# Performance work log

Hardware: AMD Instinct MI355X
Metric: run time of the kernel (lower is better)

Reference implementation:

```python
import jax, jax.numpy as jnp
import numpy as np

B, S, D = 8, 1024, 768
H = 12
DH = D // H  # 64


def setup_inputs() -> dict:
    key = jax.random.key(0)
    k1, k2 = jax.random.split(key)
    x = jax.random.normal(k1, (B, S, D), dtype=jnp.float32)
    attention_mask = jnp.zeros((B, 1, 1, S), dtype=jnp.float32)
    W = jax.random.normal(k2, (D, D), dtype=jnp.float32) * (1.0 / np.sqrt(D))
    b = jnp.zeros((D,), dtype=jnp.float32)
    return {"x": x, "attention_mask": attention_mask, "W": W, "b": b}


def reference(x, attention_mask, W, b):
    # Linear projection (torch Linear: y = x @ W^T + b; here W is [out,in])
    mixed = jnp.einsum('bsd,ed->bse', x, W) + b            # [B,S,D]
    # split heads -> [B,H,S,DH]
    xl = mixed.reshape(B, S, H, DH).transpose(0, 2, 1, 3)
    # self-attention with Q=K=V=xl
    scores = jnp.einsum('bhsd,bhtd->bhst', xl, xl) / jnp.sqrt(
        jnp.asarray(DH, dtype=xl.dtype))                    # [B,H,S,S]
    scores = scores + attention_mask
    probs = jax.nn.softmax(scores, axis=-1)
    ctx = jnp.einsum('bhst,bhtd->bhsd', probs, xl)          # [B,H,S,DH]
    ctx = ctx.transpose(0, 2, 1, 3).reshape(B, S, D)        # [B,S,D]
    return ctx
```

## Files before the change

kernel.cpp:

```cpp
#include <hip/hip_runtime.h>
#include <hip/hip_bf16.h>


#define D_MODEL 768
#define SEQ     1024
#define NHEAD   12
#define DHEAD   64
#define BATCH   8
#define QB      128
#define LOG2E   1.44269504088896f
#define FMLOG   28.8539008178f
#define SCLC    (0.125f * LOG2E)

typedef __attribute__((ext_vector_type(8)))  short bf16x8;
typedef __attribute__((ext_vector_type(4)))  short short4v;
typedef __attribute__((ext_vector_type(4)))  float f32x4;
typedef __attribute__((ext_vector_type(16))) float f32x16;

__device__ __forceinline__ unsigned short f2bf(float f) {
  __hip_bfloat16 h = __float2bfloat16(f);
  return *reinterpret_cast<unsigned short*>(&h);
}

__device__ __forceinline__ float fexp2(float x) {
#if __has_builtin(__builtin_amdgcn_exp2f)
  return __builtin_amdgcn_exp2f(x);
#else
  return exp2f(x);
#endif
}

__device__ __forceinline__ int lswz(int r, int c) {
  return (r << 6) + (c ^ ((r & 7) << 3));
}
__device__ __forceinline__ int tau(int t) {
  return (t & ~0xC) | ((t & 8) >> 1) | ((t & 4) << 1);
}

template<bool WRITE_T>
__global__ __launch_bounds__(256) void proj_kernel(
    const float* __restrict__ X, const float* __restrict__ W,
    const float* __restrict__ bias, unsigned short* __restrict__ mixed,
    unsigned short* __restrict__ mixedT)
{
  __shared__ unsigned short As[2][64 * 40];
  __shared__ unsigned short Bs[2][128 * 40];

  const int tid = threadIdx.x;
  const int l   = tid & 63;
  const int w   = tid >> 6;
  const int m0  = blockIdx.x * 64;
  const int n0  = blockIdx.y * 128;
  const int wm  = (w >> 1) * 32;
  const int wn  = (w & 1) * 64;
  const int lr  = l & 15;
  const int g   = l >> 4;
  const int lk  = g * 8;

  const int ar = tid >> 2;
  const int ac = (tid & 3) * 8;

  f32x4 a0, a1, b0[2], b1[2];
  auto loadSlab = [&](int k0) {
    const float* pa = &X[(size_t)(m0 + ar) * D_MODEL + k0 + ac];
    a0 = *(const f32x4*)pa;
    a1 = *(const f32x4*)(pa + 4);
    #pragma unroll
    for (int p = 0; p < 2; ++p) {
      const float* pb = &W[(size_t)(n0 + ar + p * 64) * D_MODEL + k0 + ac];
      b0[p] = *(const f32x4*)pb;
      b1[p] = *(const f32x4*)(pb + 4);
    }
  };
  auto stageSlab = [&](int bb) {
    bf16x8 av;
    #pragma unroll
    for (int jj = 0; jj < 4; ++jj) {
      av[jj]     = (short)f2bf(a0[jj]);
      av[4 + jj] = (short)f2bf(a1[jj]);
    }
    *(bf16x8*)&As[bb][ar * 40 + ac] = av;
    #pragma unroll
    for (int p = 0; p < 2; ++p) {
      bf16x8 bv;
      #pragma unroll
      for (int jj = 0; jj < 4; ++jj) {
        bv[jj]     = (short)f2bf(b0[p][jj]);
        bv[4 + jj] = (short)f2bf(b1[p][jj]);
      }
      *(bf16x8*)&Bs[bb][(ar + p * 64) * 40 + ac] = bv;
    }
  };

  f32x4 acc[2][4] = {};

  loadSlab(0);
  stageSlab(0);
  __syncthreads();

  int cur = 0;
  for (int k0 = 0; k0 < D_MODEL; k0 += 32) {
    const bool more = (k0 + 32 < D_MODEL);
    if (more) loadSlab(k0 + 32);

    bf16x8 af[2], bfr[4];
    #pragma unroll
    for (int am = 0; am < 2; ++am)
      af[am]  = *(const bf16x8*)&As[cur][(wm + am * 16 + lr) * 40 + lk];
    #pragma unroll
    for (int bn = 0; bn < 4; ++bn)
      bfr[bn] = *(const bf16x8*)&Bs[cur][(wn + bn * 16 + lr) * 40 + lk];

    #pragma unroll
    for (int am = 0; am < 2; ++am)
      #pragma unroll
      for (int bn = 0; bn < 4; ++bn)
        acc[am][bn] = __builtin_amdgcn_mfma_f32_16x16x32_bf16(
            af[am], bfr[bn], acc[am][bn], 0, 0, 0);

    if (more) {
      stageSlab(cur ^ 1);
      __syncthreads();
    }
    cur ^= 1;
  }

  const int orow = g * 4;
  const int bT   = m0 >> 10;
  const int tl0  = (m0 & 1023) + wm + orow;
  #pragma unroll
  for (int bn = 0; bn < 4; ++bn) {
    int   col  = n0 + wn + bn * 16 + lr;
    float bcol = bias[col];
    size_t tbase = ((size_t)bT * D_MODEL + col) * SEQ;
    #pragma unroll
    for (int am = 0; am < 2; ++am) {
      short4v pk;
      #pragma unroll
      for (int i = 0; i < 4; ++i) {
        float v = acc[am][bn][i] + bcol;
        unsigned short hv = f2bf(v);
        mixed[(size_t)(m0 + wm + am * 16 + orow + i) * D_MODEL + col] = hv;
        pk[i] = (short)hv;
      }
      if (WRITE_T)
        *(short4v*)&mixedT[tbase + tau(tl0 + am * 16)] = pk;
    }
  }
}

__global__ __launch_bounds__(256, 4) void attn_kernel(
    const unsigned short* __restrict__ mixed,
    const unsigned short* __restrict__ mixedT,
    const float* __restrict__ mask, float* __restrict__ out)
{
  __shared__ unsigned short Xbuf[2][4096];
  __shared__ unsigned short Tbuf[2][4096];
  __shared__ float maskE[SEQ];
  __shared__ float lb[128];
  __shared__ int   mflag;

  const int tid = threadIdx.x;
  const int l   = tid & 63;
  const int wq  = tid >> 6;
  const int l31 = l & 31;
  const int lh  = l >> 5;
  const int h4  = lh * 4;
  const int h8  = lh * 8;

  const int id  = blockIdx.x;
  const int xcd = id & 7;
  const int j   = id >> 3;
  const int pr  = xcd * 12 + (j >> 3);
  const int q0  = (j & 7) * QB;
  const int hd  = pr % NHEAD;
  const int b   = pr / NHEAD;

  const size_t base  = ((size_t)b * SEQ) * D_MODEL + hd * DHEAD;
  const size_t baseT = ((size_t)b * D_MODEL + hd * DHEAD) * SEQ;

  const int r0 = tid >> 3;
  const int sc = (tid & 7) * 8;

  if (tid == 0) mflag = 0;
  __syncthreads();
  {
    f32x4 mv = *(const f32x4*)&mask[(size_t)b * SEQ + tid * 4];
    #pragma unroll
    for (int jj = 0; jj < 4; ++jj)
      maskE[tid * 4 + jj] = fmaf(mv[jj], LOG2E, -FMLOG);
    if (mv[0] != 0.f || mv[1] != 0.f || mv[2] != 0.f || mv[3] != 0.f)
      mflag = 1;
  }

  unsigned short* QQ = &Xbuf[0][0];
  #pragma unroll
  for (int pp = 0; pp < 4; ++pp) {
    int g   = tid + pp * 256;
    int row = g >> 3;
    int c   = (g & 7) * 8;
    *(bf16x8*)&QQ[lswz(row, c)] =
        *(const bf16x8*)&mixed[base + (size_t)(q0 + row) * D_MODEL + c];
  }
  __syncthreads();

  const bool hm = (mflag != 0);
  bf16x8 qf[4];
  #pragma unroll
  for (int db = 0; db < 4; ++db)
    qf[db] = *(const bf16x8*)&QQ[lswz(wq * 32 + l31, db * 16 + h8)];
  __syncthreads();

  bf16x8 k0r, k1r, t0r, t1r;
  auto loadKV = [&](int tt) {
    k0r = *(const bf16x8*)&mixed[base + (size_t)(tt + r0) * D_MODEL + sc];
    k1r = *(const bf16x8*)&mixed[base + (size_t)(tt + r0 + 32) * D_MODEL + sc];
    t0r = *(const bf16x8*)&mixedT[baseT + (size_t)r0 * SEQ + tt + sc];
    t1r = *(const bf16x8*)&mixedT[baseT + (size_t)(r0 + 32) * SEQ + tt + sc];
  };
  auto stageKV = [&](unsigned short* Xd, unsigned short* Td) {
    *(bf16x8*)&Xd[lswz(r0, sc)]      = k0r;
    *(bf16x8*)&Xd[lswz(r0 + 32, sc)] = k1r;
    *(bf16x8*)&Td[lswz(r0, sc)]      = t0r;
    *(bf16x8*)&Td[lswz(r0 + 32, sc)] = t1r;
  };

  unsigned short* Xc = &Xbuf[0][0];
  unsigned short* Xn = &Xbuf[1][0];
  unsigned short* Tc = &Tbuf[0][0];
  unsigned short* Tn = &Tbuf[1][0];

  loadKV(0);
  stageKV(Xc, Tc);
  __syncthreads();

  f32x16 c0 = {}, c1 = {};
  float lsum = 0.f;

  for (int t0 = 0; t0 < SEQ; t0 += 64) {
    const bool more = (t0 + 64 < SEQ);
    if (more) loadKV(t0 + 64);

    #pragma unroll
    for (int sub = 0; sub < 2; ++sub) {
      const int sr = sub * 32;

      f32x16 s = {};
      __builtin_amdgcn_s_setprio(1);
      #pragma unroll
      for (int db = 0; db < 4; ++db) {
        bf16x8 kf = *(const bf16x8*)&Xc[lswz(sr + l31, db * 16 + h8)];
        s = __builtin_amdgcn_mfma_f32_32x32x16_bf16(kf, qf[db], s, 0, 0, 0);
      }
      __builtin_amdgcn_s_setprio(0);

      float p[16];
      if (hm) {
        #pragma unroll
        for (int r = 0; r < 16; ++r) {
          int kvr = (r & 3) + 8 * (r >> 2) + h4;
          p[r] = fexp2(fmaf(s[r], SCLC, maskE[t0 + sr + kvr]));
          lsum += p[r];
        }
      } else {
        #pragma unroll
        for (int r = 0; r < 16; ++r) {
          p[r] = fexp2(fmaf(s[r], SCLC, -FMLOG));
          lsum += p[r];
        }
      }

      __builtin_amdgcn_s_setprio(1);
      #pragma unroll
      for (int f = 0; f < 2; ++f) {
        bf16x8 pa;
        #pragma unroll
        for (int jj = 0; jj < 8; ++jj) pa[jj] = (short)f2bf(p[8 * f + jj]);
        const int cc = sr + f * 16 + h8;
        bf16x8 v0 = *(const bf16x8*)&Tc[lswz(l31, cc)];
        bf16x8 v1 = *(const bf16x8*)&Tc[lswz(32 + l31, cc)];
        c0 = __builtin_amdgcn_mfma_f32_32x32x16_bf16(pa, v0, c0, 0, 0, 0);
        c1 = __builtin_amdgcn_mfma_f32_32x32x16_bf16(pa, v1, c1, 0, 0, 0);
      }
      __builtin_amdgcn_s_setprio(0);
    }

    if (more) {
      stageKV(Xn, Tn);
      __syncthreads();
    }
    unsigned short* t;
    t = Xc; Xc = Xn; Xn = t;
    t = Tc; Tc = Tn; Tn = t;
  }

  float l_tot = lsum + __shfl_xor(lsum, 32);
  if (lh == 0) lb[wq * 32 + l31] = l_tot;

  #pragma unroll
  for (int r = 0; r < 16; ++r) {
    int qr = (r & 3) + 8 * (r >> 2) + h4;
    float linv = __builtin_amdgcn_rcpf(lb[wq * 32 + qr]);
    int row = q0 + wq * 32 + qr;
    float* orow = &out[((size_t)b * SEQ + row) * D_MODEL + hd * DHEAD];
    orow[l31]      = c0[r] * linv;
    orow[32 + l31] = c1[r] * linv;
  }
}

extern "C" void kernel_launch(void* const* d_in, const int* in_sizes, int n_in,
                              void* d_out, int out_size, void* d_ws, size_t ws_size,
                              hipStream_t stream) {
  const float* x    = (const float*)d_in[0];
  const float* mask = (const float*)d_in[1];
  const float* W    = (const float*)d_in[2];
  const float* bias = (const float*)d_in[3];
  float* out        = (float*)d_out;

  const size_t NM = (size_t)8192 * D_MODEL;
  unsigned short* mixed  = (unsigned short*)d_ws;
  unsigned short* mixedT = mixed + NM;

  dim3 gp(8192 / 64, D_MODEL / 128);
  const int nblk = (SEQ / QB) * NHEAD * BATCH;

  proj_kernel<true><<<gp, 256, 0, stream>>>(x, W, bias, mixed, mixedT);
  attn_kernel<<<nblk, 256, 0, stream>>>(mixed, mixedT, mask, out);
}
```

Baseline: 67.00 us.

## Widen projection K-slab to 64 with swizzled LDS; compute softmax denominator via MFMA

The projection GEMM now stages 64-wide K slabs in XOR-swizzled LDS instead of 32-wide padded rows, which halves the number of barriers and slab iterations and raises loads in flight per thread. Separately, the attention kernel drops the per-lane scalar row-sum and the LDS exchange of row sums. Instead it accumulates the denominator with an extra MFMA of the bf16 probabilities against a ones vector, so the sum matches the bf16-rounded probabilities used in the numerator. The cost is one more MFMA per P·V step and 16 more accumulator registers, plus more LDS in the projection kernel.

Result: slower. 76.54 us (+14.2%).

```diff
diff --git a/kernel.cpp b/kernel.cpp
--- a/kernel.cpp
+++ b/kernel.cpp
@@ -43,8 +43,8 @@
     const float* __restrict__ bias, unsigned short* __restrict__ mixed,
     unsigned short* __restrict__ mixedT)
 {
-  __shared__ unsigned short As[2][64 * 40];
-  __shared__ unsigned short Bs[2][128 * 40];
+  __shared__ unsigned short As[2][64 * 64];
+  __shared__ unsigned short Bs[2][128 * 64];
 
   const int tid = threadIdx.x;
   const int l   = tid & 63;
@@ -59,36 +59,43 @@
 
   const int ar = tid >> 2;
   const int ac = (tid & 3) * 8;
-
-  f32x4 a0, a1, b0[2], b1[2];
+  const int rb = tid >> 1;
+  const int cb = (tid & 1) * 8;
+
+  f32x4 a[4], bvr[8];
   auto loadSlab = [&](int k0) {
-    const float* pa = &X[(size_t)(m0 + ar) * D_MODEL + k0 + ac];
-    a0 = *(const f32x4*)pa;
-    a1 = *(const f32x4*)(pa + 4);
-    #pragma unroll
-    for (int p = 0; p < 2; ++p) {
-      const float* pb = &W[(size_t)(n0 + ar + p * 64) * D_MODEL + k0 + ac];
-      b0[p] = *(const f32x4*)pb;
-      b1[p] = *(const f32x4*)(pb + 4);
+    const float* pa = &X[(size_t)(m0 + ar) * D_MODEL + k0];
+    a[0] = *(const f32x4*)(pa + ac);
+    a[1] = *(const f32x4*)(pa + ac + 4);
+    a[2] = *(const f32x4*)(pa + ac + 32);
+    a[3] = *(const f32x4*)(pa + ac + 36);
+    const float* pb = &W[(size_t)(n0 + rb) * D_MODEL + k0];
+    #pragma unroll
+    for (int j = 0; j < 4; ++j) {
+      bvr[2 * j]     = *(const f32x4*)(pb + cb + j * 16);
+      bvr[2 * j + 1] = *(const f32x4*)(pb + cb + j * 16 + 4);
     }
   };
   auto stageSlab = [&](int bb) {
-    bf16x8 av;
-    #pragma unroll
-    for (int jj = 0; jj < 4; ++jj) {
-      av[jj]     = (short)f2bf(a0[jj]);
-      av[4 + jj] = (short)f2bf(a1[jj]);
-    }
-    *(bf16x8*)&As[bb][ar * 40 + ac] = av;
-    #pragma unroll
-    for (int p = 0; p < 2; ++p) {
+    #pragma unroll
+    for (int h = 0; h < 2; ++h) {
+      bf16x8 av;
+      #pragma unroll
+      for (int jj = 0; jj < 4; ++jj) {
+        av[jj]     = (short)f2bf(a[2 * h][jj]);
+        av[4 + jj] = (short)f2bf(a[2 * h + 1][jj]);
+      }
+      *(bf16x8*)&As[bb][lswz(ar, ac + h * 32)] = av;
+    }
+    #pragma unroll
+    for (int j = 0; j < 4; ++j) {
       bf16x8 bv;
       #pragma unroll
       for (int jj = 0; jj < 4; ++jj) {
-        bv[jj]     = (short)f2bf(b0[p][jj]);
-        bv[4 + jj] = (short)f2bf(b1[p][jj]);
-      }
-      *(bf16x8*)&Bs[bb][(ar + p * 64) * 40 + ac] = bv;
+        bv[jj]     = (short)f2bf(bvr[2 * j][jj]);
+        bv[4 + jj] = (short)f2bf(bvr[2 * j + 1][jj]);
+      }
+      *(bf16x8*)&Bs[bb][lswz(rb, cb + j * 16)] = bv;
     }
   };
 
@@ -99,24 +106,28 @@
   __syncthreads();
 
   int cur = 0;
-  for (int k0 = 0; k0 < D_MODEL; k0 += 32) {
-    const bool more = (k0 + 32 < D_MODEL);
-    if (more) loadSlab(k0 + 32);
-
-    bf16x8 af[2], bfr[4];
-    #pragma unroll
-    for (int am = 0; am < 2; ++am)
-      af[am]  = *(const bf16x8*)&As[cur][(wm + am * 16 + lr) * 40 + lk];
-    #pragma unroll
-    for (int bn = 0; bn < 4; ++bn)
-      bfr[bn] = *(const bf16x8*)&Bs[cur][(wn + bn * 16 + lr) * 40 + lk];
-
-    #pragma unroll
-    for (int am = 0; am < 2; ++am)
+  for (int k0 = 0; k0 < D_MODEL; k0 += 64) {
+    const bool more = (k0 + 64 < D_MODEL);
+    if (more) loadSlab(k0 + 64);
+
+    #pragma unroll
+    for (int kk = 0; kk < 2; ++kk) {
+      const int kc = kk * 32 + lk;
+      bf16x8 af[2], bfr[4];
+      #pragma unroll
+      for (int am = 0; am < 2; ++am)
+        af[am]  = *(const bf16x8*)&As[cur][lswz(wm + am * 16 + lr, kc)];
       #pragma unroll
       for (int bn = 0; bn < 4; ++bn)
-        acc[am][bn] = __builtin_amdgcn_mfma_f32_16x16x32_bf16(
-            af[am], bfr[bn], acc[am][bn], 0, 0, 0);
+        bfr[bn] = *(const bf16x8*)&Bs[cur][lswz(wn + bn * 16 + lr, kc)];
+
+      #pragma unroll
+      for (int am = 0; am < 2; ++am)
+        #pragma unroll
+        for (int bn = 0; bn < 4; ++bn)
+          acc[am][bn] = __builtin_amdgcn_mfma_f32_16x16x32_bf16(
+              af[am], bfr[bn], acc[am][bn], 0, 0, 0);
+    }
 
     if (more) {
       stageSlab(cur ^ 1);
@@ -157,7 +168,6 @@
   __shared__ unsigned short Xbuf[2][4096];
   __shared__ unsigned short Tbuf[2][4096];
   __shared__ float maskE[SEQ];
-  __shared__ float lb[128];
   __shared__ int   mflag;
 
   const int tid = threadIdx.x;
@@ -234,8 +244,11 @@
   stageKV(Xc, Tc);
   __syncthreads();
 
-  f32x16 c0 = {}, c1 = {};
-  float lsum = 0.f;
+  bf16x8 onesf;
+  #pragma unroll
+  for (int jj = 0; jj < 8; ++jj) onesf[jj] = (short)0x3F80;
+
+  f32x16 c0 = {}, c1 = {}, lacc = {};
 
   for (int t0 = 0; t0 < SEQ; t0 += 64) {
     const bool more = (t0 + 64 < SEQ);
@@ -260,14 +273,11 @@
         for (int r = 0; r < 16; ++r) {
           int kvr = (r & 3) + 8 * (r >> 2) + h4;
           p[r] = fexp2(fmaf(s[r], SCLC, maskE[t0 + sr + kvr]));
-          lsum += p[r];
         }
       } else {
         #pragma unroll
-        for (int r = 0; r < 16; ++r) {
+        for (int r = 0; r < 16; ++r)
           p[r] = fexp2(fmaf(s[r], SCLC, -FMLOG));
-          lsum += p[r];
-        }
       }
 
       __builtin_amdgcn_s_setprio(1);
@@ -279,8 +289,9 @@
         const int cc = sr + f * 16 + h8;
         bf16x8 v0 = *(const bf16x8*)&Tc[lswz(l31, cc)];
         bf16x8 v1 = *(const bf16x8*)&Tc[lswz(32 + l31, cc)];
-        c0 = __builtin_amdgcn_mfma_f32_32x32x16_bf16(pa, v0, c0, 0, 0, 0);
-        c1 = __builtin_amdgcn_mfma_f32_32x32x16_bf16(pa, v1, c1, 0, 0, 0);
+        c0   = __builtin_amdgcn_mfma_f32_32x32x16_bf16(pa, v0, c0, 0, 0, 0);
+        c1   = __builtin_amdgcn_mfma_f32_32x32x16_bf16(pa, v1, c1, 0, 0, 0);
+        lacc = __builtin_amdgcn_mfma_f32_32x32x16_bf16(pa, onesf, lacc, 0, 0, 0);
       }
       __builtin_amdgcn_s_setprio(0);
     }
@@ -294,13 +305,10 @@
     t = Tc; Tc = Tn; Tn = t;
   }
 
-  float l_tot = lsum + __shfl_xor(lsum, 32);
-  if (lh == 0) lb[wq * 32 + l31] = l_tot;
-
   #pragma unroll
   for (int r = 0; r < 16; ++r) {
-    int qr = (r & 3) + 8 * (r >> 2) + h4;
-    float linv = __builtin_amdgcn_rcpf(lb[wq * 32 + qr]);
+    float linv = __builtin_amdgcn_rcpf(lacc[r]);
+    int qr  = (r & 3) + 8 * (r >> 2) + h4;
     int row = q0 + wq * 32 + qr;
     float* orow = &out[((size_t)b * SEQ + row) * D_MODEL + hd * DHEAD];
     orow[l31]      = c0[r] * linv;
```
